# Kernel tuning notes

Hardware: AMD Instinct MI355X
Metric: run time of the kernel (lower is better)

## Reference

```python
import jax, jax.numpy as jnp
import numpy as np

B, D = 16384, 1024
N_CROSS = 3
EPS = 1e-3  # keras BatchNormalization default epsilon


def _bn(x, gamma, beta, mean, var):
    # inference-mode batch norm over feature axis
    return gamma * (x - mean) * jax.lax.rsqrt(var + EPS) + beta


def setup_inputs() -> dict:
    key = jax.random.key(0)
    ks = jax.random.split(key, 16)
    s = lambda fan_in: 1.0 / np.sqrt(fan_in)
    inp = {
        "x": jax.random.normal(ks[0], (B, D), jnp.float32),
        "cross_w": jax.random.normal(ks[1], (N_CROSS, D), jnp.float32) * s(D),
        "cross_b": jax.random.normal(ks[2], (N_CROSS, D), jnp.float32) * 0.01,
        "w1": jax.random.normal(ks[3], (D, 64), jnp.float32) * s(D),
        "b1": jnp.zeros((64,), jnp.float32),
        "gamma1": jnp.ones((64,), jnp.float32),
        "beta1": jnp.zeros((64,), jnp.float32),
        "mean1": jax.random.normal(ks[4], (64,), jnp.float32) * 0.1,
        "var1": jax.random.uniform(ks[5], (64,), jnp.float32, 0.5, 1.5),
        "w2": jax.random.normal(ks[6], (64, 48), jnp.float32) * s(64),
        "b2": jnp.zeros((48,), jnp.float32),
        "gamma2": jnp.ones((48,), jnp.float32),
        "beta2": jnp.zeros((48,), jnp.float32),
        "mean2": jax.random.normal(ks[7], (48,), jnp.float32) * 0.1,
        "var2": jax.random.uniform(ks[8], (48,), jnp.float32, 0.5, 1.5),
        "w3": jax.random.normal(ks[9], (48, 24), jnp.float32) * s(48),
        "b3": jnp.zeros((24,), jnp.float32),
        "gamma3": jnp.ones((24,), jnp.float32),
        "beta3": jnp.zeros((24,), jnp.float32),
        "mean3": jax.random.normal(ks[10], (24,), jnp.float32) * 0.1,
        "var3": jax.random.uniform(ks[11], (24,), jnp.float32, 0.5, 1.5),
        "w_out": jax.random.normal(ks[12], (D + 24, 1), jnp.float32) * s(D + 24),
        "b_out": jnp.zeros((1,), jnp.float32),
    }
    return inp


def reference(x, cross_w, cross_b, w1, b1, gamma1, beta1, mean1, var1,
              w2, b2, gamma2, beta2, mean2, var2,
              w3, b3, gamma3, beta3, mean3, var3, w_out, b_out):
    # ---- cross network: xl = x0 * (xl . w) + b + xl ----
    # Algebraically identical to matmul(x0[:,:,None], xl[:,None,:]) @ w,
    # computed in O(B*D) instead of materializing [B, D, D].
    x0 = x
    xl = x
    for i in range(N_CROSS):
        scal = jnp.einsum('bd,d->b', xl, cross_w[i])  # [B]
        xl = x0 * scal[:, None] + cross_b[i] + xl
    # ---- deep tower (inference: dropout is identity, BN uses moving stats) ----
    h = _bn(jax.nn.relu(x @ w1 + b1), gamma1, beta1, mean1, var1)
    h = _bn(jnp.tanh(h @ w2 + b2), gamma2, beta2, mean2, var2)
    h = _bn(jnp.tanh(h @ w3 + b3), gamma3, beta3, mean3, var3)
    out = jnp.concatenate([xl, h], axis=1)           # [B, D+24]
    return jax.nn.sigmoid(out @ w_out + b_out)       # [B, 1]
```

## Files before the change

### kernel.cpp

```cpp
#include <hip/hip_runtime.h>
#include <hip/hip_bf16.h>
#include <math.h>

typedef __attribute__((ext_vector_type(8))) short bf16x8;
typedef __attribute__((ext_vector_type(4))) float f32x4;

constexpr int BD = 1024;
constexpr float EPS = 1e-3f;
constexpr int WB_MAIN = 32 * 5 * 64 * 8 * 2;
constexpr int WB2_OFF = WB_MAIN;
constexpr int WB3_OFF = WB2_OFF + 6144;
constexpr int CST_OFF = WB3_OFF + 4096;

__device__ __forceinline__ float wave_allsum(float v) {
#pragma unroll
    for (int m = 1; m < 64; m <<= 1) v += __shfl_xor(v, m, 64);
    return v;
}
__device__ __forceinline__ unsigned short f2bf(float f) {
    __hip_bfloat16 h = __float2bfloat16(f);
    unsigned short u; __builtin_memcpy(&u, &h, 2);
    return u;
}
__device__ __forceinline__ float bf2f(unsigned short u) {
    return __uint_as_float(((unsigned)u) << 16);
}
__device__ __forceinline__ unsigned cvt_pk_bf16(float lo, float hi) {
    unsigned r;
    asm("v_cvt_pk_bf16_f32 %0, %1, %2" : "=v"(r) : "v"(lo), "v"(hi));
    return r;
}
__device__ __forceinline__ float tanh_fast(float x) {
    const float xc = fminf(fmaxf(x, -15.f), 15.f);
    const float e = __expf(2.f * xc);
    return (e - 1.f) * __builtin_amdgcn_rcpf(e + 1.f);
}
__device__ __forceinline__ float sigmoid_fast(float z) {
    return __builtin_amdgcn_rcpf(1.f + __expf(-z));
}

__global__ void dcn_prep(const float* __restrict__ w1,
                         const float* __restrict__ cross_w,
                         const float* __restrict__ cross_b,
                         const float* __restrict__ w_out,
                         const float* __restrict__ w2,
                         const float* __restrict__ w3,
                         unsigned short* __restrict__ ws) {
    const int bx = blockIdx.x;
    if (bx == 40) {
        if (threadIdx.x < 64) {
            const int l = threadIdx.x;
            float q2 = 0.f, q3 = 0.f, Cc = 0.f;
            for (int j = 0; j < 16; ++j) {
                const int k = l * 16 + j;
                const float c0 = cross_b[k], c1 = cross_b[BD + k], c2 = cross_b[2 * BD + k];
                q2 += c0 * cross_w[BD + k];
                q3 += (c0 + c1) * cross_w[2 * BD + k];
                Cc += (c0 + c1 + c2) * w_out[k];
            }
            q2 = wave_allsum(q2); q3 = wave_allsum(q3); Cc = wave_allsum(Cc);
            float* consts = (float*)((char*)ws + CST_OFF);
            if (l == 0) { consts[0] = q2; consts[1] = q3; consts[2] = Cc; }
        }
        return;
    }
    if (bx < 40) {
        const int idx = bx * 256 + threadIdx.x;
        const int g = idx / 320;
        const int rem = idx - g * 320;
        const int t = rem >> 6;
        const int l = rem & 63;
        const int c = l & 15;
        const int k0 = g * 32 + (l >> 4) * 8;
        unsigned short o[8] __attribute__((aligned(16)));
#pragma unroll
        for (int j = 0; j < 8; ++j) {
            const int k = k0 + j;
            unsigned short r;
            if (t < 4) {
                r = f2bf(w1[k * 64 + t * 16 + c]);
            } else if (c < 8) {
                const int vsel = c & 3;
                const float v = (vsel < 3) ? cross_w[vsel * BD + k] : w_out[k];
                const unsigned short h = f2bf(v);
                r = (c < 4) ? h : f2bf(v - bf2f(h));
            } else {
                r = 0;
            }
            o[j] = r;
        }
        *(uint4*)(ws + (size_t)idx * 8) = *(const uint4*)o;
        return;
    }
    const int slot = (bx - 41) * 256 + threadIdx.x;
    if (slot < 384) {
        const int f = slot >> 6, l = slot & 63;
        const int K = f / 3, T = f % 3;
        const int kb = K * 32 + (l >> 4) * 8;
        const int col = T * 16 + (l & 15);
        unsigned short o[8] __attribute__((aligned(16)));
#pragma unroll
        for (int j = 0; j < 8; ++j) o[j] = f2bf(w2[(kb + j) * 48 + col]);
        unsigned short* wb2 = (unsigned short*)((char*)ws + WB2_OFF);
        *(uint4*)(wb2 + (size_t)slot * 8) = *(const uint4*)o;
    } else if (slot < 640) {
        const int s2 = slot - 384;
        const int f = s2 >> 6, l = s2 & 63;
        const int K = f >> 1, T = f & 1;
        const int kb = K * 32 + (l >> 4) * 8;
        const int col = T * 16 + (l & 15);
        unsigned short o[8] __attribute__((aligned(16)));
#pragma unroll
        for (int j = 0; j < 8; ++j) {
            const int k = kb + j;
            o[j] = (k < 48 && col < 24) ? f2bf(w3[k * 24 + col]) : (unsigned short)0;
        }
        unsigned short* wb3 = (unsigned short*)((char*)ws + WB3_OFF);
        *(uint4*)(wb3 + (size_t)s2 * 8) = *(const uint4*)o;
    }
}

__global__ __launch_bounds__(128, 2) void dcn_main(
    const float* __restrict__ x,
    const unsigned short* __restrict__ wbm,
    const unsigned short* __restrict__ w2f,
    const unsigned short* __restrict__ w3f,
    const float* __restrict__ consts,
    const float* __restrict__ b1, const float* __restrict__ g1,
    const float* __restrict__ be1, const float* __restrict__ m1, const float* __restrict__ v1,
    const float* __restrict__ b2, const float* __restrict__ g2,
    const float* __restrict__ be2, const float* __restrict__ m2, const float* __restrict__ v2,
    const float* __restrict__ b3, const float* __restrict__ g3,
    const float* __restrict__ be3, const float* __restrict__ m3, const float* __restrict__ v3,
    const float* __restrict__ w_out, const float* __restrict__ b_out,
    float* __restrict__ out)
{
    __shared__ char sb[14336] __attribute__((aligned(16)));
    constexpr int RED = 0, H1 = 5120, H2 = 9472, LC = 13824;

    const int tid = threadIdx.x;
    const int l = tid & 63;
    const int w = tid >> 6;
    const int ar = l & 15;
    const int ag = l >> 4;
    const int gr0 = blockIdx.x * 16;

    const float* xbase = x + (size_t)(gr0 + ar) * BD + w * 512 + ag * 8;
    const bf16x8* bb = (const bf16x8*)wbm + (size_t)(w * 16 * 5) * 64 + l;

    float4 A0[8], A1[8];
#pragma unroll
    for (int s = 0; s < 8; ++s) {
        A0[s] = *(const float4*)(xbase + s * 32);
        A1[s] = *(const float4*)(xbase + s * 32 + 4);
    }
    bf16x8 Bf[4][5];
#pragma unroll
    for (int s = 0; s < 4; ++s)
#pragma unroll
        for (int t = 0; t < 5; ++t) Bf[s][t] = bb[(s * 5 + t) * 64];

    f32x4 acc0 = {0.f,0.f,0.f,0.f}, acc1 = acc0, acc2 = acc0, acc3 = acc0, acc4 = acc0;

#pragma unroll
    for (int s = 0; s < 16; ++s) {
        const float4 va0 = A0[s & 7];
        const float4 va1 = A1[s & 7];
        if (s < 8) {
            A0[s & 7] = *(const float4*)(xbase + (s + 8) * 32);
            A1[s & 7] = *(const float4*)(xbase + (s + 8) * 32 + 4);
        }
        const bf16x8 B0 = Bf[s & 3][0], B1 = Bf[s & 3][1], B2 = Bf[s & 3][2],
                     B3 = Bf[s & 3][3], B4 = Bf[s & 3][4];
        if (s + 4 < 16) {
#pragma unroll
            for (int t = 0; t < 5; ++t) Bf[s & 3][t] = bb[((s + 4) * 5 + t) * 64];
        }
        union { unsigned u[4]; bf16x8 v; } XH, XL;
        XH.u[0] = cvt_pk_bf16(va0.x, va0.y);
        XH.u[1] = cvt_pk_bf16(va0.z, va0.w);
        XH.u[2] = cvt_pk_bf16(va1.x, va1.y);
        XH.u[3] = cvt_pk_bf16(va1.z, va1.w);
        const float l0 = va0.x - __uint_as_float(XH.u[0] << 16);
        const float l1 = va0.y - __uint_as_float(XH.u[0] & 0xFFFF0000u);
        const float l2 = va0.z - __uint_as_float(XH.u[1] << 16);
        const float l3 = va0.w - __uint_as_float(XH.u[1] & 0xFFFF0000u);
        const float l4 = va1.x - __uint_as_float(XH.u[2] << 16);
        const float l5 = va1.y - __uint_as_float(XH.u[2] & 0xFFFF0000u);
        const float l6 = va1.z - __uint_as_float(XH.u[3] << 16);
        const float l7 = va1.w - __uint_as_float(XH.u[3] & 0xFFFF0000u);
        XL.u[0] = cvt_pk_bf16(l0, l1);
        XL.u[1] = cvt_pk_bf16(l2, l3);
        XL.u[2] = cvt_pk_bf16(l4, l5);
        XL.u[3] = cvt_pk_bf16(l6, l7);

        acc0 = __builtin_amdgcn_mfma_f32_16x16x32_bf16(XH.v, B0, acc0, 0, 0, 0);
        acc1 = __builtin_amdgcn_mfma_f32_16x16x32_bf16(XH.v, B1, acc1, 0, 0, 0);
        acc2 = __builtin_amdgcn_mfma_f32_16x16x32_bf16(XH.v, B2, acc2, 0, 0, 0);
        acc3 = __builtin_amdgcn_mfma_f32_16x16x32_bf16(XH.v, B3, acc3, 0, 0, 0);
        acc4 = __builtin_amdgcn_mfma_f32_16x16x32_bf16(XH.v, B4, acc4, 0, 0, 0);
        acc4 = __builtin_amdgcn_mfma_f32_16x16x32_bf16(XL.v, B4, acc4, 0, 0, 0);
    }

    if (w == 1) {
        *(f32x4*)&sb[RED + 0 * 1024 + l * 16] = acc0;
        *(f32x4*)&sb[RED + 1 * 1024 + l * 16] = acc1;
        *(f32x4*)&sb[RED + 2 * 1024 + l * 16] = acc2;
        *(f32x4*)&sb[RED + 3 * 1024 + l * 16] = acc3;
        *(f32x4*)&sb[RED + 4 * 1024 + l * 16] = acc4;
    }
    __syncthreads();
    if (w == 1) return;

    acc0 += *(const f32x4*)&sb[RED + 0 * 1024 + l * 16];
    acc1 += *(const f32x4*)&sb[RED + 1 * 1024 + l * 16];
    acc2 += *(const f32x4*)&sb[RED + 2 * 1024 + l * 16];
    acc3 += *(const f32x4*)&sb[RED + 3 * 1024 + l * 16];
    acc4 += *(const f32x4*)&sb[RED + 4 * 1024 + l * 16];

    const bf16x8* w2b = (const bf16x8*)w2f + l;
    bf16x8 W2[6];
#pragma unroll
    for (int f = 0; f < 6; ++f) W2[f] = w2b[f * 64];
    const bf16x8* w3b = (const bf16x8*)w3f + l;
    bf16x8 W3[4];
#pragma unroll
    for (int f = 0; f < 4; ++f) W3[f] = w3b[f * 64];

    const float q2c = consts[0], q3c = consts[1], Ccc = consts[2];
    const float bo = b_out[0];
    const float wo0 = w_out[1024 + ar];
    const float wo1 = (ar < 8) ? w_out[1040 + ar] : 0.f;
    float b1p[4], g1p[4], be1p[4], m1p[4], iv1p[4];
#pragma unroll
    for (int t = 0; t < 4; ++t) {
        const int c = t * 16 + ar;
        b1p[t] = b1[c]; g1p[t] = g1[c]; be1p[t] = be1[c]; m1p[t] = m1[c];
        iv1p[t] = rsqrtf(v1[c] + EPS);
    }
    float b2p[3], g2p[3], be2p[3], m2p[3], iv2p[3];
#pragma unroll
    for (int t = 0; t < 3; ++t) {
        const int c = t * 16 + ar;
        b2p[t] = b2[c]; g2p[t] = g2[c]; be2p[t] = be2[c]; m2p[t] = m2[c];
        iv2p[t] = rsqrtf(v2[c] + EPS);
    }
    float b3p[2], g3p[2], be3p[2], m3p[2], iv3p[2];
#pragma unroll
    for (int t = 0; t < 2; ++t) {
        const int c = t == 0 ? ar : (16 + ar < 24 ? 16 + ar : 23);
        b3p[t] = b3[c]; g3p[t] = g3[c]; be3p[t] = be3[c]; m3p[t] = m3[c];
        iv3p[t] = rsqrtf(v3[c] + EPS);
    }

    {
        f32x4 p4 = acc4;
#pragma unroll
        for (int q = 0; q < 4; ++q) p4[q] += __shfl_xor(acc4[q], 4, 64);
        if (ar < 4) {
#pragma unroll
            for (int q = 0; q < 4; ++q)
                *(float*)&sb[LC + ((ag * 4 + q) * 4 + ar) * 4] = p4[q];
        }
    }

    {
        const f32x4 av[4] = {acc0, acc1, acc2, acc3};
#pragma unroll
        for (int t = 0; t < 4; ++t) {
            const int c = t * 16 + ar;
#pragma unroll
            for (int q = 0; q < 4; ++q) {
                const float y = fmaxf(av[t][q] + b1p[t], 0.f);
                const float h = fmaf(g1p[t] * (y - m1p[t]), iv1p[t], be1p[t]);
                *(float*)&sb[H1 + (ag * 4 + q) * 272 + c * 4] = h;
            }
        }
    }
    {
        const f32x4 z4 = {0.f, 0.f, 0.f, 0.f};
        *(f32x4*)&sb[H2 + ar * 272 + 192 + ag * 16] = z4;
    }

    bf16x8 a2[2];
#pragma unroll
    for (int K = 0; K < 2; ++K) {
        const float4 f0 = *(const float4*)&sb[H1 + ar * 272 + (K * 32 + ag * 8) * 4];
        const float4 f1 = *(const float4*)&sb[H1 + ar * 272 + (K * 32 + ag * 8) * 4 + 16];
        union { unsigned u[4]; bf16x8 v; } P;
        P.u[0] = cvt_pk_bf16(f0.x, f0.y);
        P.u[1] = cvt_pk_bf16(f0.z, f0.w);
        P.u[2] = cvt_pk_bf16(f1.x, f1.y);
        P.u[3] = cvt_pk_bf16(f1.z, f1.w);
        a2[K] = P.v;
    }
    f32x4 c2t[3] = {{0.f,0.f,0.f,0.f},{0.f,0.f,0.f,0.f},{0.f,0.f,0.f,0.f}};
#pragma unroll
    for (int K = 0; K < 2; ++K) {
        c2t[0] = __builtin_amdgcn_mfma_f32_16x16x32_bf16(a2[K], W2[K * 3 + 0], c2t[0], 0, 0, 0);
        c2t[1] = __builtin_amdgcn_mfma_f32_16x16x32_bf16(a2[K], W2[K * 3 + 1], c2t[1], 0, 0, 0);
        c2t[2] = __builtin_amdgcn_mfma_f32_16x16x32_bf16(a2[K], W2[K * 3 + 2], c2t[2], 0, 0, 0);
    }
#pragma unroll
    for (int t = 0; t < 3; ++t) {
        const int c = t * 16 + ar;
#pragma unroll
        for (int q = 0; q < 4; ++q) {
            const float th = tanh_fast(c2t[t][q] + b2p[t]);
            const float h = fmaf(g2p[t] * (th - m2p[t]), iv2p[t], be2p[t]);
            *(float*)&sb[H2 + (ag * 4 + q) * 272 + c * 4] = h;
        }
    }

    bf16x8 a3[2];
#pragma unroll
    for (int K = 0; K < 2; ++K) {
        const float4 f0 = *(const float4*)&sb[H2 + ar * 272 + (K * 32 + ag * 8) * 4];
        const float4 f1 = *(const float4*)&sb[H2 + ar * 272 + (K * 32 + ag * 8) * 4 + 16];
        union { unsigned u[4]; bf16x8 v; } P;
        P.u[0] = cvt_pk_bf16(f0.x, f0.y);
        P.u[1] = cvt_pk_bf16(f0.z, f0.w);
        P.u[2] = cvt_pk_bf16(f1.x, f1.y);
        P.u[3] = cvt_pk_bf16(f1.z, f1.w);
        a3[K] = P.v;
    }
    f32x4 c3t[2] = {{0.f,0.f,0.f,0.f},{0.f,0.f,0.f,0.f}};
#pragma unroll
    for (int K = 0; K < 2; ++K) {
        c3t[0] = __builtin_amdgcn_mfma_f32_16x16x32_bf16(a3[K], W3[K * 2 + 0], c3t[0], 0, 0, 0);
        c3t[1] = __builtin_amdgcn_mfma_f32_16x16x32_bf16(a3[K], W3[K * 2 + 1], c3t[1], 0, 0, 0);
    }
    float contrib[4];
#pragma unroll
    for (int q = 0; q < 4; ++q) {
        const float t0 = tanh_fast(c3t[0][q] + b3p[0]);
        const float h0 = fmaf(g3p[0] * (t0 - m3p[0]), iv3p[0], be3p[0]);
        const float t1 = tanh_fast(c3t[1][q] + b3p[1]);
        const float h1v = fmaf(g3p[1] * (t1 - m3p[1]), iv3p[1], be3p[1]);
        contrib[q] = h0 * wo0 + h1v * wo1;
    }
#pragma unroll
    for (int m = 1; m < 16; m <<= 1) {
#pragma unroll
        for (int q = 0; q < 4; ++q) contrib[q] += __shfl_xor(contrib[q], m, 64);
    }

#pragma unroll
    for (int q = 0; q < 4; ++q) {
        const f32x4 pr = *(const f32x4*)&sb[LC + (ag * 4 + q) * 16];
        const float p1 = pr[0], p2 = pr[1], p3 = pr[2], d0 = pr[3];
        const float s1 = p1;
        const float s2 = fmaf(1.f + s1, p2, q2c);
        const float s3 = fmaf(1.f + s1 + s2, p3, q3c);
        const float alpha = 1.f + s1 + s2 + s3;
        const float z = fmaf(alpha, d0, Ccc) + contrib[q] + bo;
        const float o = sigmoid_fast(z);
        if (ar == q) out[gr0 + ag * 4 + q] = o;
    }
}

extern "C" void kernel_launch(void* const* d_in, const int* in_sizes, int n_in,
                              void* d_out, int out_size, void* d_ws, size_t ws_size,
                              hipStream_t stream) {
    const float* x       = (const float*)d_in[0];
    const float* cross_w = (const float*)d_in[1];
    const float* cross_b = (const float*)d_in[2];
    const float* w1      = (const float*)d_in[3];
    const float* b1      = (const float*)d_in[4];
    const float* g1      = (const float*)d_in[5];
    const float* be1     = (const float*)d_in[6];
    const float* m1      = (const float*)d_in[7];
    const float* v1      = (const float*)d_in[8];
    const float* w2      = (const float*)d_in[9];
    const float* b2      = (const float*)d_in[10];
    const float* g2      = (const float*)d_in[11];
    const float* be2     = (const float*)d_in[12];
    const float* m2      = (const float*)d_in[13];
    const float* v2      = (const float*)d_in[14];
    const float* w3      = (const float*)d_in[15];
    const float* b3      = (const float*)d_in[16];
    const float* g3      = (const float*)d_in[17];
    const float* be3     = (const float*)d_in[18];
    const float* m3      = (const float*)d_in[19];
    const float* v3      = (const float*)d_in[20];
    const float* w_out   = (const float*)d_in[21];
    const float* b_out   = (const float*)d_in[22];
    float* out = (float*)d_out;

    unsigned short* ws = (unsigned short*)d_ws;
    const unsigned short* w2f = (const unsigned short*)((char*)d_ws + WB2_OFF);
    const unsigned short* w3f = (const unsigned short*)((char*)d_ws + WB3_OFF);
    const float* consts = (const float*)((char*)d_ws + CST_OFF);

    dcn_prep<<<44, 256, 0, stream>>>(w1, cross_w, cross_b, w_out, w2, w3, ws);
    dcn_main<<<1024, 128, 0, stream>>>(x, ws, w2f, w3f, consts,
                                       b1, g1, be1, m1, v1,
                                       b2, g2, be2, m2, v2,
                                       b3, g3, be3, m3, v3,
                                       w_out, b_out, out);
}
```

Before: 26.02 us.

## Stage x tiles into swizzled LDS via global_load_lds instead of register prefetch

Replaces the register-held double buffer of x rows with direct global-to-LDS asynchronous loads (global_load_lds) into a 64KB shared buffer, using an XOR swizzle to avoid bank conflicts. All four chunks are issued up front, and the main loop reads A fragments from LDS. This frees vector registers and lets more loads be in flight. In exchange, LDS use per block grows to 64KB, which can limit occupancy below the launch_bounds target of 2 blocks. The waitcnt only guards the first chunk, so later chunks appear to rely on implicit ordering, which risks races.

```diff
diff --git a/kernel.cpp b/kernel.cpp
--- a/kernel.cpp
+++ b/kernel.cpp
@@ -4,6 +4,9 @@
 
 typedef __attribute__((ext_vector_type(8))) short bf16x8;
 typedef __attribute__((ext_vector_type(4))) float f32x4;
+
+#define AS3 __attribute__((address_space(3)))
+#define AS1 __attribute__((address_space(1)))
 
 constexpr int BD = 1024;
 constexpr float EPS = 1e-3f;
@@ -135,8 +138,8 @@
     const float* __restrict__ w_out, const float* __restrict__ b_out,
     float* __restrict__ out)
 {
-    __shared__ char sb[14336] __attribute__((aligned(16)));
-    constexpr int RED = 0, H1 = 5120, H2 = 9472, LC = 13824;
+    __shared__ char sb[65536] __attribute__((aligned(16)));
+    constexpr int RED = 32768, H1 = 37888, H2 = 42240, LC = 46592;
 
     const int tid = threadIdx.x;
     const int l = tid & 63;
@@ -144,62 +147,85 @@
     const int ar = l & 15;
     const int ag = l >> 4;
     const int gr0 = blockIdx.x * 16;
-
-    const float* xbase = x + (size_t)(gr0 + ar) * BD + w * 512 + ag * 8;
+    const int wbase = w * 32768;
+
+    const int srow = l >> 5;
+    const int scb = (l & 31) * 16;
+    const char* xrow = (const char*)x + (size_t)(gr0 + srow) * 4096 + (size_t)w * 2048;
+
+#define STAGE(c) do {                                                                    \
+    char* lb_ = &sb[wbase + (c) * 8192];                                                 \
+    _Pragma("unroll")                                                                    \
+    for (int i_ = 0; i_ < 8; ++i_) {                                                     \
+        const int r7_ = ((i_ << 1) + srow) & 7;                                          \
+        const char* g_ = xrow + (size_t)i_ * 8192 + (c) * 512 + (scb ^ (r7_ << 4));      \
+        __builtin_amdgcn_global_load_lds((AS1 const void*)g_,                            \
+                                         (AS3 void*)(lb_ + i_ * 1024), 16, 0, 0);        \
+    }                                                                                    \
+} while (0)
+
+    STAGE(0);
+    STAGE(1);
+    STAGE(2);
+    STAGE(3);
+    __builtin_amdgcn_sched_barrier(0);
+#undef STAGE
+
     const bf16x8* bb = (const bf16x8*)wbm + (size_t)(w * 16 * 5) * 64 + l;
-
-    float4 A0[8], A1[8];
-#pragma unroll
-    for (int s = 0; s < 8; ++s) {
-        A0[s] = *(const float4*)(xbase + s * 32);
-        A1[s] = *(const float4*)(xbase + s * 32 + 4);
-    }
     bf16x8 Bf[4][5];
 #pragma unroll
     for (int s = 0; s < 4; ++s)
 #pragma unroll
         for (int t = 0; t < 5; ++t) Bf[s][t] = bb[(s * 5 + t) * 64];
+    __builtin_amdgcn_sched_barrier(0);
+    asm volatile("s_waitcnt vmcnt(20)" ::: "memory");
+    __builtin_amdgcn_sched_barrier(0);
 
     f32x4 acc0 = {0.f,0.f,0.f,0.f}, acc1 = acc0, acc2 = acc0, acc3 = acc0, acc4 = acc0;
 
-#pragma unroll
-    for (int s = 0; s < 16; ++s) {
-        const float4 va0 = A0[s & 7];
-        const float4 va1 = A1[s & 7];
-        if (s < 8) {
-            A0[s & 7] = *(const float4*)(xbase + (s + 8) * 32);
-            A1[s & 7] = *(const float4*)(xbase + (s + 8) * 32 + 4);
-        }
-        const bf16x8 B0 = Bf[s & 3][0], B1 = Bf[s & 3][1], B2 = Bf[s & 3][2],
-                     B3 = Bf[s & 3][3], B4 = Bf[s & 3][4];
-        if (s + 4 < 16) {
-#pragma unroll
-            for (int t = 0; t < 5; ++t) Bf[s & 3][t] = bb[((s + 4) * 5 + t) * 64];
-        }
-        union { unsigned u[4]; bf16x8 v; } XH, XL;
-        XH.u[0] = cvt_pk_bf16(va0.x, va0.y);
-        XH.u[1] = cvt_pk_bf16(va0.z, va0.w);
-        XH.u[2] = cvt_pk_bf16(va1.x, va1.y);
-        XH.u[3] = cvt_pk_bf16(va1.z, va1.w);
-        const float l0 = va0.x - __uint_as_float(XH.u[0] << 16);
-        const float l1 = va0.y - __uint_as_float(XH.u[0] & 0xFFFF0000u);
-        const float l2 = va0.z - __uint_as_float(XH.u[1] << 16);
-        const float l3 = va0.w - __uint_as_float(XH.u[1] & 0xFFFF0000u);
-        const float l4 = va1.x - __uint_as_float(XH.u[2] << 16);
-        const float l5 = va1.y - __uint_as_float(XH.u[2] & 0xFFFF0000u);
-        const float l6 = va1.z - __uint_as_float(XH.u[3] << 16);
-        const float l7 = va1.w - __uint_as_float(XH.u[3] & 0xFFFF0000u);
-        XL.u[0] = cvt_pk_bf16(l0, l1);
-        XL.u[1] = cvt_pk_bf16(l2, l3);
-        XL.u[2] = cvt_pk_bf16(l4, l5);
-        XL.u[3] = cvt_pk_bf16(l6, l7);
-
-        acc0 = __builtin_amdgcn_mfma_f32_16x16x32_bf16(XH.v, B0, acc0, 0, 0, 0);
-        acc1 = __builtin_amdgcn_mfma_f32_16x16x32_bf16(XH.v, B1, acc1, 0, 0, 0);
-        acc2 = __builtin_amdgcn_mfma_f32_16x16x32_bf16(XH.v, B2, acc2, 0, 0, 0);
-        acc3 = __builtin_amdgcn_mfma_f32_16x16x32_bf16(XH.v, B3, acc3, 0, 0, 0);
-        acc4 = __builtin_amdgcn_mfma_f32_16x16x32_bf16(XH.v, B4, acc4, 0, 0, 0);
-        acc4 = __builtin_amdgcn_mfma_f32_16x16x32_bf16(XL.v, B4, acc4, 0, 0, 0);
+    const int swz = (ar & 7) << 4;
+    const int arb = ar * 512;
+
+#pragma unroll
+    for (int c = 0; c < 4; ++c) {
+        const int bufo = wbase + c * 8192;
+#pragma unroll
+        for (int s4 = 0; s4 < 4; ++s4) {
+            const int s = c * 4 + s4;
+            const int cb0 = s4 * 128 + ag * 32;
+            const float4 va0 = *(const float4*)&sb[bufo + arb + (cb0 ^ swz)];
+            const float4 va1 = *(const float4*)&sb[bufo + arb + ((cb0 + 16) ^ swz)];
+            const bf16x8 B0 = Bf[s & 3][0], B1 = Bf[s & 3][1], B2 = Bf[s & 3][2],
+                         B3 = Bf[s & 3][3], B4 = Bf[s & 3][4];
+            if (s + 4 < 16) {
+#pragma unroll
+                for (int t = 0; t < 5; ++t) Bf[s & 3][t] = bb[((s + 4) * 5 + t) * 64];
+            }
+            union { unsigned u[4]; bf16x8 v; } XH, XL;
+            XH.u[0] = cvt_pk_bf16(va0.x, va0.y);
+            XH.u[1] = cvt_pk_bf16(va0.z, va0.w);
+            XH.u[2] = cvt_pk_bf16(va1.x, va1.y);
+            XH.u[3] = cvt_pk_bf16(va1.z, va1.w);
+            const float l0 = va0.x - __uint_as_float(XH.u[0] << 16);
+            const float l1 = va0.y - __uint_as_float(XH.u[0] & 0xFFFF0000u);
+            const float l2 = va0.z - __uint_as_float(XH.u[1] << 16);
+            const float l3 = va0.w - __uint_as_float(XH.u[1] & 0xFFFF0000u);
+            const float l4 = va1.x - __uint_as_float(XH.u[2] << 16);
+            const float l5 = va1.y - __uint_as_float(XH.u[2] & 0xFFFF0000u);
+            const float l6 = va1.z - __uint_as_float(XH.u[3] << 16);
+            const float l7 = va1.w - __uint_as_float(XH.u[3] & 0xFFFF0000u);
+            XL.u[0] = cvt_pk_bf16(l0, l1);
+            XL.u[1] = cvt_pk_bf16(l2, l3);
+            XL.u[2] = cvt_pk_bf16(l4, l5);
+            XL.u[3] = cvt_pk_bf16(l6, l7);
+
+            acc0 = __builtin_amdgcn_mfma_f32_16x16x32_bf16(XH.v, B0, acc0, 0, 0, 0);
+            acc1 = __builtin_amdgcn_mfma_f32_16x16x32_bf16(XH.v, B1, acc1, 0, 0, 0);
+            acc2 = __builtin_amdgcn_mfma_f32_16x16x32_bf16(XH.v, B2, acc2, 0, 0, 0);
+            acc3 = __builtin_amdgcn_mfma_f32_16x16x32_bf16(XH.v, B3, acc3, 0, 0, 0);
+            acc4 = __builtin_amdgcn_mfma_f32_16x16x32_bf16(XH.v, B4, acc4, 0, 0, 0);
+            acc4 = __builtin_amdgcn_mfma_f32_16x16x32_bf16(XL.v, B4, acc4, 0, 0, 0);
+        }
     }
 
     if (w == 1) {
```

Result: slower. 30.34 us (+16.6%).

## Process 32 rows per block, reuse B fragments across two row tiles, split epilogue

Applied to the files above, without the earlier changes.

Each block now handles 32 rows instead of 16. Every weight fragment loaded from global memory feeds MFMAs for two row tiles, which halves weight traffic per row. After the K-split reduction the two waves exchange partial sums through LDS, and each wave then runs the deep-tower epilogue for its own 16 rows, so no wave sits idle as wave 1 did before. The grid drops to 512 blocks and LDS per block doubles. Register pressure rises from the doubled accumulators, and the shorter prefetch depth plus fewer blocks may reduce latency hiding.

```diff
diff --git a/kernel.cpp b/kernel.cpp
--- a/kernel.cpp
+++ b/kernel.cpp
@@ -135,88 +135,125 @@
     const float* __restrict__ w_out, const float* __restrict__ b_out,
     float* __restrict__ out)
 {
-    __shared__ char sb[14336] __attribute__((aligned(16)));
-    constexpr int RED = 0, H1 = 5120, H2 = 9472, LC = 13824;
+    __shared__ char sb[28160] __attribute__((aligned(16)));
 
     const int tid = threadIdx.x;
     const int l = tid & 63;
     const int w = tid >> 6;
     const int ar = l & 15;
     const int ag = l >> 4;
-    const int gr0 = blockIdx.x * 16;
-
-    const float* xbase = x + (size_t)(gr0 + ar) * BD + w * 512 + ag * 8;
+    const int gr0 = blockIdx.x * 32;
+
+    const int H1 = 10240 + w * 4352;
+    const int H2 = 18944 + w * 4352;
+    const int LC = 27648 + w * 256;
+
+    const float* xb0 = x + (size_t)(gr0 + ar) * BD + w * 512 + ag * 8;
+    const float* xb1 = xb0 + (size_t)16 * BD;
+
     const bf16x8* bb = (const bf16x8*)wbm + (size_t)(w * 16 * 5) * 64 + l;
 
-    float4 A0[8], A1[8];
-#pragma unroll
-    for (int s = 0; s < 8; ++s) {
-        A0[s] = *(const float4*)(xbase + s * 32);
-        A1[s] = *(const float4*)(xbase + s * 32 + 4);
-    }
-    bf16x8 Bf[4][5];
-#pragma unroll
-    for (int s = 0; s < 4; ++s)
+    float4 Aa0[4], Aa1[4], Ab0[4], Ab1[4];
+#pragma unroll
+    for (int s = 0; s < 4; ++s) {
+        Aa0[s] = *(const float4*)(xb0 + s * 32);
+        Aa1[s] = *(const float4*)(xb0 + s * 32 + 4);
+        Ab0[s] = *(const float4*)(xb1 + s * 32);
+        Ab1[s] = *(const float4*)(xb1 + s * 32 + 4);
+    }
+    bf16x8 Bf[2][5];
+#pragma unroll
+    for (int s = 0; s < 2; ++s)
 #pragma unroll
         for (int t = 0; t < 5; ++t) Bf[s][t] = bb[(s * 5 + t) * 64];
 
-    f32x4 acc0 = {0.f,0.f,0.f,0.f}, acc1 = acc0, acc2 = acc0, acc3 = acc0, acc4 = acc0;
+    f32x4 z4 = {0.f,0.f,0.f,0.f};
+    f32x4 a0 = z4, a1 = z4, a2_ = z4, a3_ = z4, a4 = z4;
+    f32x4 b0 = z4, b1_ = z4, b2_ = z4, b3_ = z4, b4 = z4;
+
+#define CVTPAIR(VA0, VA1, XH, XL) do {                                          \
+    XH.u[0] = cvt_pk_bf16(VA0.x, VA0.y);                                        \
+    XH.u[1] = cvt_pk_bf16(VA0.z, VA0.w);                                        \
+    XH.u[2] = cvt_pk_bf16(VA1.x, VA1.y);                                        \
+    XH.u[3] = cvt_pk_bf16(VA1.z, VA1.w);                                        \
+    const float t0_ = VA0.x - __uint_as_float(XH.u[0] << 16);                   \
+    const float t1_ = VA0.y - __uint_as_float(XH.u[0] & 0xFFFF0000u);           \
+    const float t2_ = VA0.z - __uint_as_float(XH.u[1] << 16);                   \
+    const float t3_ = VA0.w - __uint_as_float(XH.u[1] & 0xFFFF0000u);           \
+    const float t4_ = VA1.x - __uint_as_float(XH.u[2] << 16);                   \
+    const float t5_ = VA1.y - __uint_as_float(XH.u[2] & 0xFFFF0000u);           \
+    const float t6_ = VA1.z - __uint_as_float(XH.u[3] << 16);                   \
+    const float t7_ = VA1.w - __uint_as_float(XH.u[3] & 0xFFFF0000u);           \
+    XL.u[0] = cvt_pk_bf16(t0_, t1_);                                            \
+    XL.u[1] = cvt_pk_bf16(t2_, t3_);                                            \
+    XL.u[2] = cvt_pk_bf16(t4_, t5_);                                            \
+    XL.u[3] = cvt_pk_bf16(t6_, t7_);                                            \
+} while (0)
 
 #pragma unroll
     for (int s = 0; s < 16; ++s) {
-        const float4 va0 = A0[s & 7];
-        const float4 va1 = A1[s & 7];
-        if (s < 8) {
-            A0[s & 7] = *(const float4*)(xbase + (s + 8) * 32);
-            A1[s & 7] = *(const float4*)(xbase + (s + 8) * 32 + 4);
-        }
-        const bf16x8 B0 = Bf[s & 3][0], B1 = Bf[s & 3][1], B2 = Bf[s & 3][2],
-                     B3 = Bf[s & 3][3], B4 = Bf[s & 3][4];
-        if (s + 4 < 16) {
-#pragma unroll
-            for (int t = 0; t < 5; ++t) Bf[s & 3][t] = bb[((s + 4) * 5 + t) * 64];
-        }
-        union { unsigned u[4]; bf16x8 v; } XH, XL;
-        XH.u[0] = cvt_pk_bf16(va0.x, va0.y);
-        XH.u[1] = cvt_pk_bf16(va0.z, va0.w);
-        XH.u[2] = cvt_pk_bf16(va1.x, va1.y);
-        XH.u[3] = cvt_pk_bf16(va1.z, va1.w);
-        const float l0 = va0.x - __uint_as_float(XH.u[0] << 16);
-        const float l1 = va0.y - __uint_as_float(XH.u[0] & 0xFFFF0000u);
-        const float l2 = va0.z - __uint_as_float(XH.u[1] << 16);
-        const float l3 = va0.w - __uint_as_float(XH.u[1] & 0xFFFF0000u);
-        const float l4 = va1.x - __uint_as_float(XH.u[2] << 16);
-        const float l5 = va1.y - __uint_as_float(XH.u[2] & 0xFFFF0000u);
-        const float l6 = va1.z - __uint_as_float(XH.u[3] << 16);
-        const float l7 = va1.w - __uint_as_float(XH.u[3] & 0xFFFF0000u);
-        XL.u[0] = cvt_pk_bf16(l0, l1);
-        XL.u[1] = cvt_pk_bf16(l2, l3);
-        XL.u[2] = cvt_pk_bf16(l4, l5);
-        XL.u[3] = cvt_pk_bf16(l6, l7);
-
-        acc0 = __builtin_amdgcn_mfma_f32_16x16x32_bf16(XH.v, B0, acc0, 0, 0, 0);
-        acc1 = __builtin_amdgcn_mfma_f32_16x16x32_bf16(XH.v, B1, acc1, 0, 0, 0);
-        acc2 = __builtin_amdgcn_mfma_f32_16x16x32_bf16(XH.v, B2, acc2, 0, 0, 0);
-        acc3 = __builtin_amdgcn_mfma_f32_16x16x32_bf16(XH.v, B3, acc3, 0, 0, 0);
-        acc4 = __builtin_amdgcn_mfma_f32_16x16x32_bf16(XH.v, B4, acc4, 0, 0, 0);
-        acc4 = __builtin_amdgcn_mfma_f32_16x16x32_bf16(XL.v, B4, acc4, 0, 0, 0);
-    }
-
-    if (w == 1) {
-        *(f32x4*)&sb[RED + 0 * 1024 + l * 16] = acc0;
-        *(f32x4*)&sb[RED + 1 * 1024 + l * 16] = acc1;
-        *(f32x4*)&sb[RED + 2 * 1024 + l * 16] = acc2;
-        *(f32x4*)&sb[RED + 3 * 1024 + l * 16] = acc3;
-        *(f32x4*)&sb[RED + 4 * 1024 + l * 16] = acc4;
+        const float4 va0 = Aa0[s & 3], va1 = Aa1[s & 3];
+        const float4 vb0 = Ab0[s & 3], vb1 = Ab1[s & 3];
+        if (s < 12) {
+            Aa0[s & 3] = *(const float4*)(xb0 + (s + 4) * 32);
+            Aa1[s & 3] = *(const float4*)(xb0 + (s + 4) * 32 + 4);
+            Ab0[s & 3] = *(const float4*)(xb1 + (s + 4) * 32);
+            Ab1[s & 3] = *(const float4*)(xb1 + (s + 4) * 32 + 4);
+        }
+        const bf16x8 B0 = Bf[s & 1][0], B1 = Bf[s & 1][1], B2 = Bf[s & 1][2],
+                     B3 = Bf[s & 1][3], B4 = Bf[s & 1][4];
+        if (s + 2 < 16) {
+#pragma unroll
+            for (int t = 0; t < 5; ++t) Bf[s & 1][t] = bb[((s + 2) * 5 + t) * 64];
+        }
+        union { unsigned u[4]; bf16x8 v; } XHa, XLa, XHb, XLb;
+        CVTPAIR(va0, va1, XHa, XLa);
+        CVTPAIR(vb0, vb1, XHb, XLb);
+
+        a0  = __builtin_amdgcn_mfma_f32_16x16x32_bf16(XHa.v, B0, a0, 0, 0, 0);
+        b0  = __builtin_amdgcn_mfma_f32_16x16x32_bf16(XHb.v, B0, b0, 0, 0, 0);
+        a1  = __builtin_amdgcn_mfma_f32_16x16x32_bf16(XHa.v, B1, a1, 0, 0, 0);
+        b1_ = __builtin_amdgcn_mfma_f32_16x16x32_bf16(XHb.v, B1, b1_, 0, 0, 0);
+        a2_ = __builtin_amdgcn_mfma_f32_16x16x32_bf16(XHa.v, B2, a2_, 0, 0, 0);
+        b2_ = __builtin_amdgcn_mfma_f32_16x16x32_bf16(XHb.v, B2, b2_, 0, 0, 0);
+        a3_ = __builtin_amdgcn_mfma_f32_16x16x32_bf16(XHa.v, B3, a3_, 0, 0, 0);
+        b3_ = __builtin_amdgcn_mfma_f32_16x16x32_bf16(XHb.v, B3, b3_, 0, 0, 0);
+        a4  = __builtin_amdgcn_mfma_f32_16x16x32_bf16(XHa.v, B4, a4, 0, 0, 0);
+        a4  = __builtin_amdgcn_mfma_f32_16x16x32_bf16(XLa.v, B4, a4, 0, 0, 0);
+        b4  = __builtin_amdgcn_mfma_f32_16x16x32_bf16(XHb.v, B4, b4, 0, 0, 0);
+        b4  = __builtin_amdgcn_mfma_f32_16x16x32_bf16(XLb.v, B4, b4, 0, 0, 0);
+    }
+#undef CVTPAIR
+
+    const int pkMine = w * 5120;
+    const int pkOther = 5120 - pkMine;
+    if (w == 0) {
+        *(f32x4*)&sb[pkMine + 0 * 1024 + l * 16] = b0;
+        *(f32x4*)&sb[pkMine + 1 * 1024 + l * 16] = b1_;
+        *(f32x4*)&sb[pkMine + 2 * 1024 + l * 16] = b2_;
+        *(f32x4*)&sb[pkMine + 3 * 1024 + l * 16] = b3_;
+        *(f32x4*)&sb[pkMine + 4 * 1024 + l * 16] = b4;
+    } else {
+        *(f32x4*)&sb[pkMine + 0 * 1024 + l * 16] = a0;
+        *(f32x4*)&sb[pkMine + 1 * 1024 + l * 16] = a1;
+        *(f32x4*)&sb[pkMine + 2 * 1024 + l * 16] = a2_;
+        *(f32x4*)&sb[pkMine + 3 * 1024 + l * 16] = a3_;
+        *(f32x4*)&sb[pkMine + 4 * 1024 + l * 16] = a4;
     }
     __syncthreads();
-    if (w == 1) return;
-
-    acc0 += *(const f32x4*)&sb[RED + 0 * 1024 + l * 16];
-    acc1 += *(const f32x4*)&sb[RED + 1 * 1024 + l * 16];
-    acc2 += *(const f32x4*)&sb[RED + 2 * 1024 + l * 16];
-    acc3 += *(const f32x4*)&sb[RED + 3 * 1024 + l * 16];
-    acc4 += *(const f32x4*)&sb[RED + 4 * 1024 + l * 16];
+    f32x4 acc0, acc1, acc2, acc3, acc4;
+    if (w == 0) {
+        acc0 = a0;  acc1 = a1;  acc2 = a2_; acc3 = a3_; acc4 = a4;
+    } else {
+        acc0 = b0;  acc1 = b1_; acc2 = b2_; acc3 = b3_; acc4 = b4;
+    }
+    acc0 += *(const f32x4*)&sb[pkOther + 0 * 1024 + l * 16];
+    acc1 += *(const f32x4*)&sb[pkOther + 1 * 1024 + l * 16];
+    acc2 += *(const f32x4*)&sb[pkOther + 2 * 1024 + l * 16];
+    acc3 += *(const f32x4*)&sb[pkOther + 3 * 1024 + l * 16];
+    acc4 += *(const f32x4*)&sb[pkOther + 4 * 1024 + l * 16];
+
+    const int myrow0 = gr0 + w * 16;
 
     const bf16x8* w2b = (const bf16x8*)w2f + l;
     bf16x8 W2[6];
@@ -278,11 +315,10 @@
         }
     }
     {
-        const f32x4 z4 = {0.f, 0.f, 0.f, 0.f};
         *(f32x4*)&sb[H2 + ar * 272 + 192 + ag * 16] = z4;
     }
 
-    bf16x8 a2[2];
+    bf16x8 a2f[2];
 #pragma unroll
     for (int K = 0; K < 2; ++K) {
         const float4 f0 = *(const float4*)&sb[H1 + ar * 272 + (K * 32 + ag * 8) * 4];
@@ -292,14 +328,14 @@
         P.u[1] = cvt_pk_bf16(f0.z, f0.w);
         P.u[2] = cvt_pk_bf16(f1.x, f1.y);
         P.u[3] = cvt_pk_bf16(f1.z, f1.w);
-        a2[K] = P.v;
-    }
-    f32x4 c2t[3] = {{0.f,0.f,0.f,0.f},{0.f,0.f,0.f,0.f},{0.f,0.f,0.f,0.f}};
+        a2f[K] = P.v;
+    }
+    f32x4 c2t[3] = {z4, z4, z4};
 #pragma unroll
     for (int K = 0; K < 2; ++K) {
-        c2t[0] = __builtin_amdgcn_mfma_f32_16x16x32_bf16(a2[K], W2[K * 3 + 0], c2t[0], 0, 0, 0);
-        c2t[1] = __builtin_amdgcn_mfma_f32_16x16x32_bf16(a2[K], W2[K * 3 + 1], c2t[1], 0, 0, 0);
-        c2t[2] = __builtin_amdgcn_mfma_f32_16x16x32_bf16(a2[K], W2[K * 3 + 2], c2t[2], 0, 0, 0);
+        c2t[0] = __builtin_amdgcn_mfma_f32_16x16x32_bf16(a2f[K], W2[K * 3 + 0], c2t[0], 0, 0, 0);
+        c2t[1] = __builtin_amdgcn_mfma_f32_16x16x32_bf16(a2f[K], W2[K * 3 + 1], c2t[1], 0, 0, 0);
+        c2t[2] = __builtin_amdgcn_mfma_f32_16x16x32_bf16(a2f[K], W2[K * 3 + 2], c2t[2], 0, 0, 0);
     }
 #pragma unroll
     for (int t = 0; t < 3; ++t) {
@@ -312,7 +348,7 @@
         }
     }
 
-    bf16x8 a3[2];
+    bf16x8 a3f[2];
 #pragma unroll
     for (int K = 0; K < 2; ++K) {
         const float4 f0 = *(const float4*)&sb[H2 + ar * 272 + (K * 32 + ag * 8) * 4];
@@ -322,13 +358,13 @@
         P.u[1] = cvt_pk_bf16(f0.z, f0.w);
         P.u[2] = cvt_pk_bf16(f1.x, f1.y);
         P.u[3] = cvt_pk_bf16(f1.z, f1.w);
-        a3[K] = P.v;
-    }
-    f32x4 c3t[2] = {{0.f,0.f,0.f,0.f},{0.f,0.f,0.f,0.f}};
+        a3f[K] = P.v;
+    }
+    f32x4 c3t[2] = {z4, z4};
 #pragma unroll
     for (int K = 0; K < 2; ++K) {
-        c3t[0] = __builtin_amdgcn_mfma_f32_16x16x32_bf16(a3[K], W3[K * 2 + 0], c3t[0], 0, 0, 0);
-        c3t[1] = __builtin_amdgcn_mfma_f32_16x16x32_bf16(a3[K], W3[K * 2 + 1], c3t[1], 0, 0, 0);
+        c3t[0] = __builtin_amdgcn_mfma_f32_16x16x32_bf16(a3f[K], W3[K * 2 + 0], c3t[0], 0, 0, 0);
+        c3t[1] = __builtin_amdgcn_mfma_f32_16x16x32_bf16(a3f[K], W3[K * 2 + 1], c3t[1], 0, 0, 0);
     }
     float contrib[4];
 #pragma unroll
@@ -355,7 +391,7 @@
         const float alpha = 1.f + s1 + s2 + s3;
         const float z = fmaf(alpha, d0, Ccc) + contrib[q] + bo;
         const float o = sigmoid_fast(z);
-        if (ar == q) out[gr0 + ag * 4 + q] = o;
+        if (ar == q) out[myrow0 + ag * 4 + q] = o;
     }
 }
 
@@ -393,9 +429,9 @@
     const float* consts = (const float*)((char*)d_ws + CST_OFF);
 
     dcn_prep<<<44, 256, 0, stream>>>(w1, cross_w, cross_b, w_out, w2, w3, ws);
-    dcn_main<<<1024, 128, 0, stream>>>(x, ws, w2f, w3f, consts,
-                                       b1, g1, be1, m1, v1,
-                                       b2, g2, be2, m2, v2,
-                                       b3, g3, be3, m3, v3,
-                                       w_out, b_out, out);
-}
+    dcn_main<<<512, 128, 0, stream>>>(x, ws, w2f, w3f, consts,
+                                      b1, g1, be1, m1, v1,
+                                      b2, g2, be2, m2, v2,
+                                      b3, g3, be3, m3, v3,
+                                      w_out, b_out, out);
+}
```

Result: no change. 25.73 us (median of 2 runs) (-1.1%).
